# Kernel optimization log

Hardware: AMD Instinct MI355X
Metric: run time of the kernel (lower is better)

The kernel has to match this reference:

```python
import jax, jax.numpy as jnp
import numpy as np

B, N, D, D_MODEL = 4, 2048, 512, 512


def setup_inputs() -> dict:
    key = jax.random.key(0)
    kx, kq, kk, kv, ks = jax.random.split(key, 5)
    scale = 1.0 / np.sqrt(D)
    x = jax.random.normal(kx, (B, N, D), dtype=jnp.float32)
    Wq = (jax.random.normal(kq, (D, D_MODEL), dtype=jnp.float32) * scale)
    Wk = (jax.random.normal(kk, (D, D_MODEL), dtype=jnp.float32) * scale)
    Wv = (jax.random.normal(kv, (D, D_MODEL), dtype=jnp.float32) * scale)
    Ws = (jax.random.normal(ks, (D, 1), dtype=jnp.float32) * scale)
    return {"x": x, "Wq": Wq, "Wk": Wk, "Wv": Wv, "Ws": Ws}


def reference(x, Wq, Wk, Wv, Ws):
    # Projections (Linear, no bias)
    Q = x @ Wq                      # (B, N, d_model)
    K = x @ Wk                      # (B, N, d_model)
    V = x @ Wv                      # (B, N, d_model)
    sigma = x @ Ws                  # (B, N, 1)

    n = x.shape[1]
    dm = Wq.shape[1]

    # Prior association: Gaussian kernel over |i-j| distance, row-normalized
    idx = jnp.arange(n)
    dist = jnp.abs(idx[:, None] - idx[None, :]).astype(x.dtype)      # (N, N)
    inv_norm = 1.0 / (jnp.sqrt(2.0 * jnp.pi).astype(x.dtype) * jnp.abs(sigma))
    gaussian = inv_norm * jnp.exp(-0.5 * jnp.square(dist[None] / sigma))  # (B,N,N)
    P = gaussian / jnp.sum(gaussian, axis=-1, keepdims=True)

    # Series association: scaled dot-product softmax attention
    scores = jnp.einsum('bnd,bmd->bnm', Q, K) / jnp.sqrt(jnp.asarray(dm, x.dtype))
    S = jax.nn.softmax(scores, axis=-1)                               # (B,N,N)

    # Reconstruction
    Z = S @ V                                                          # (B,N,d_model)
    return (Z, P)
```

## Files before the change

### kernel.cpp

```cpp
#include <hip/hip_runtime.h>

typedef float f32x4 __attribute__((ext_vector_type(4)));
typedef short s16x8 __attribute__((ext_vector_type(8)));
typedef unsigned short us4 __attribute__((ext_vector_type(4)));

#define MFMA16(a, b, c) __builtin_amdgcn_mfma_f32_16x16x32_bf16(a, b, c, 0, 0, 0)

#define GLOAD_LDS16(gp, lp) __builtin_amdgcn_global_load_lds( \
    (__attribute__((address_space(1))) void*)(gp),            \
    (__attribute__((address_space(3))) void*)(lp), 16, 0, 0)

__device__ __forceinline__ unsigned short f2bf(float f) {
    union { float f; unsigned u; } v; v.f = f;
    unsigned r = v.u + 0x7fffu + ((v.u >> 16) & 1u);
    return (unsigned short)(r >> 16);
}

__device__ __forceinline__ void gemm_core256(
    const unsigned short* __restrict__ Ab, size_t Astride,
    const unsigned short* __restrict__ Bb, size_t Bstride,
    int K, unsigned short* sh, int t, f32x4 acc[8][4])
{
    const int w = t >> 6, lane = t & 63;
    const int c = lane & 15, quad = lane >> 4;
    const int arow = (w >> 2) * 128;
    const int brow = (w & 3) * 64;
    const int srow = t >> 2;
    const int scol = (t & 3) * 8;

    const unsigned short* ga = Ab + (size_t)srow * Astride + scol;
    const unsigned short* gb = Bb + (size_t)srow * Bstride + scol;
    const int ntil = K >> 5;

#define STAGE256(p, bbuf) do {                                      \
        unsigned short* nb = sh + (bbuf) * 16384;                   \
        int kk = (p) * 32;                                          \
        GLOAD_LDS16(ga + kk,                 nb + t * 8);           \
        GLOAD_LDS16(ga + kk + 128 * Astride, nb + 4096 + t * 8);    \
        GLOAD_LDS16(gb + kk,                 nb + 8192 + t * 8);    \
        GLOAD_LDS16(gb + kk + 128 * Bstride, nb + 12288 + t * 8);   \
    } while (0)

    STAGE256(0, 0);
    STAGE256(1, 1);

    int cur = 0;
    for (int i = 0; i < ntil; i++) {
        if (i + 1 < ntil) asm volatile("s_waitcnt vmcnt(4)" ::: "memory");
        else              asm volatile("s_waitcnt vmcnt(0)" ::: "memory");
        __builtin_amdgcn_s_barrier();
        __builtin_amdgcn_sched_barrier(0);

        const unsigned short* buf = sh + cur * 16384;
        s16x8 af[8], bf[4];
        #pragma unroll
        for (int q = 0; q < 8; q++)
            af[q] = *(const s16x8*)(buf + (arow + q * 16 + c) * 32 + quad * 8);
        #pragma unroll
        for (int q = 0; q < 4; q++)
            bf[q] = *(const s16x8*)(buf + 8192 + (brow + q * 16 + c) * 32 + quad * 8);

        asm volatile("s_waitcnt lgkmcnt(0)" ::: "memory");
        __builtin_amdgcn_sched_barrier(0);

        #pragma unroll
        for (int mt = 0; mt < 8; mt++)
            #pragma unroll
            for (int nt = 0; nt < 4; nt++)
                acc[mt][nt] = MFMA16(af[mt], bf[nt], acc[mt][nt]);

        __builtin_amdgcn_s_barrier();
        __builtin_amdgcn_sched_barrier(0);

        if (i + 2 < ntil) STAGE256(i + 2, cur);
        cur ^= 1;
    }
#undef STAGE256
}

__device__ __forceinline__ void prior_wave(
    const float* __restrict__ x, const float* __restrict__ wsv,
    float* __restrict__ pout, int row, int lane)
{
    const float4* xr = (const float4*)(x + (size_t)row * 512);
    const float4* wr = (const float4*)wsv;
    float4 a0 = xr[lane * 2],     b0 = wr[lane * 2];
    float4 a1 = xr[lane * 2 + 1], b1 = wr[lane * 2 + 1];
    float part = a0.x * b0.x + a0.y * b0.y + a0.z * b0.z + a0.w * b0.w
               + a1.x * b1.x + a1.y * b1.y + a1.z * b1.z + a1.w * b1.w;
    #pragma unroll
    for (int o = 32; o; o >>= 1) part += __shfl_xor(part, o, 64);
    float sigma = part;
    float inv2 = 0.5f / (sigma * sigma);

    int i = row & 2047;
    float g[32];
    float sum = 0.f;
    #pragma unroll
    for (int u = 0; u < 8; u++) {
        #pragma unroll
        for (int v = 0; v < 4; v++) {
            float d = (float)(u * 256 + lane * 4 + v - i);
            float e = __expf(-(d * d) * inv2);
            g[u * 4 + v] = e;
            sum += e;
        }
    }
    #pragma unroll
    for (int o = 32; o; o >>= 1) sum += __shfl_xor(sum, o, 64);
    float inv = 1.0f / sum;

    float4* pr = (float4*)(pout + (size_t)row * 2048);
    #pragma unroll
    for (int u = 0; u < 8; u++) {
        float4 o4 = { g[u * 4] * inv, g[u * 4 + 1] * inv,
                      g[u * 4 + 2] * inv, g[u * 4 + 3] * inv };
        pr[u * 64 + lane] = o4;
    }
}

__global__ __launch_bounds__(256) void k_convert(
    const float* __restrict__ x, const float* __restrict__ wq,
    const float* __restrict__ wk, const float* __restrict__ wv,
    unsigned short* __restrict__ xbf, unsigned short* __restrict__ wt)
{
    __shared__ __align__(16) unsigned short lt[64][72];

    int bid = blockIdx.x, t = threadIdx.x;
    if (bid < 4096) {
        int gid = bid * 256 + t;
        float4 v = ((const float4*)x)[gid];
        us4 o = { f2bf(v.x), f2bf(v.y), f2bf(v.z), f2bf(v.w) };
        ((us4*)xbf)[gid] = o;
    } else {
        int idx = bid - 4096;
        int w = idx >> 6;
        int tile = idx & 63;
        int tk = tile >> 3, tn = tile & 7;
        const float* src = ((w == 0) ? wq : (w == 1) ? wk : wv)
                         + (size_t)(tk * 64) * 512 + tn * 64;

        int row = t >> 2;
        int c0 = (t & 3) * 16;
        const float4* s = (const float4*)(src + (size_t)row * 512 + c0);
        #pragma unroll
        for (int q = 0; q < 4; q++) {
            float4 v = s[q];
            lt[c0 + q * 4 + 0][row] = f2bf(v.x);
            lt[c0 + q * 4 + 1][row] = f2bf(v.y);
            lt[c0 + q * 4 + 2][row] = f2bf(v.z);
            lt[c0 + q * 4 + 3][row] = f2bf(v.w);
        }
        __syncthreads();

        int n = t >> 2;
        int k0 = (t & 3) * 16;
        s16x8 a = *(const s16x8*)&lt[n][k0];
        s16x8 b = *(const s16x8*)&lt[n][k0 + 8];
        unsigned short* dst = wt + (((size_t)(w * 512 + tn * 64 + n)) << 9)
                                 + tk * 64 + k0;
        *(s16x8*)dst = a;
        *(s16x8*)(dst + 8) = b;
    }
}

__global__ __launch_bounds__(512, 2) void k_proj(
    const unsigned short* __restrict__ xbf, const unsigned short* __restrict__ wt,
    unsigned short* __restrict__ qbf, unsigned short* __restrict__ kbf,
    unsigned short* __restrict__ vtbf)
{
    __shared__ __align__(16) unsigned short sh[32768];

    int t = threadIdx.x;
    int mt_ = blockIdx.x / 6, nt_ = blockIdx.x % 6;
    int m0 = mt_ * 256, n0 = nt_ * 256;

    f32x4 acc[8][4] = {};
    gemm_core256(xbf + (size_t)m0 * 512, 512, wt + (size_t)n0 * 512, 512,
                 512, sh, t, acc);

    int w = t >> 6, lane = t & 63, c = lane & 15, quad = lane >> 4;
    int wr = w >> 2, wc = w & 3;
    int sel = nt_ >> 1;

    if (sel < 2) {
        unsigned short* dst = sel ? kbf : qbf;
        int ncol0 = n0 - sel * 512;
        #pragma unroll
        for (int mt = 0; mt < 8; mt++) {
            #pragma unroll
            for (int nt = 0; nt < 4; nt++) {
                int col = ncol0 + wc * 64 + nt * 16 + c;
                #pragma unroll
                for (int r = 0; r < 4; r++) {
                    int rw = m0 + wr * 128 + mt * 16 + quad * 4 + r;
                    dst[(size_t)rw * 512 + col] = f2bf(acc[mt][nt][r]);
                }
            }
        }
    } else {
        #pragma unroll
        for (int mt = 0; mt < 8; mt++) {
            int rw0 = m0 + wr * 128 + mt * 16 + quad * 4;
            int bb = rw0 >> 11, nn = rw0 & 2047;
            #pragma unroll
            for (int nt = 0; nt < 4; nt++) {
                int d = (n0 - 1024) + wc * 64 + nt * 16 + c;
                us4 pk = { f2bf(acc[mt][nt][0]), f2bf(acc[mt][nt][1]),
                           f2bf(acc[mt][nt][2]), f2bf(acc[mt][nt][3]) };
                *(us4*)(vtbf + ((size_t)(bb * 512 + d)) * 2048 + nn) = pk;
            }
        }
    }
}

__device__ __forceinline__ void score_body(
    const unsigned short* __restrict__ qbf, const unsigned short* __restrict__ kbf,
    unsigned short* __restrict__ pbf,
    int b, int m0, int n0, int t, unsigned short* sh)
{
    f32x4 acc[8][4] = {};
    gemm_core256(qbf + (size_t)(b * 2048 + m0) * 512, 512,
                 kbf + (size_t)(b * 2048 + n0) * 512, 512,
                 512, sh, t, acc);

    int w = t >> 6, lane = t & 63, c = lane & 15, quad = lane >> 4;
    int wr = w >> 2, wc = w & 3;
    const float scale = 0.044194173824159216f;

    #pragma unroll
    for (int mt = 0; mt < 8; mt++) {
        #pragma unroll
        for (int nt = 0; nt < 4; nt++) {
            int col = n0 + wc * 64 + nt * 16 + c;
            #pragma unroll
            for (int r = 0; r < 4; r++) {
                int row = m0 + wr * 128 + mt * 16 + quad * 4 + r;
                pbf[(size_t)(b * 2048 + row) * 2048 + col]
                    = f2bf(__expf(acc[mt][nt][r] * scale));
            }
        }
    }
}

__global__ __launch_bounds__(512, 2) void k_score_prior(
    const unsigned short* __restrict__ qbf, const unsigned short* __restrict__ kbf,
    unsigned short* __restrict__ pbf,
    const float* __restrict__ x, const float* __restrict__ wsv,
    float* __restrict__ pout)
{
    __shared__ __align__(16) unsigned short sh[32768];

    int bid = blockIdx.x, t = threadIdx.x;
    if (bid < 256) {
        int b = bid >> 6, r = bid & 63;
        score_body(qbf, kbf, pbf, b, ((r >> 3) & 7) * 256, (r & 7) * 256, t, sh);
    } else {
        int row = (bid - 256) * 8 + (t >> 6);
        prior_wave(x, wsv, pout, row, t & 63);
    }
}

__global__ __launch_bounds__(512, 2) void k_score(
    const unsigned short* __restrict__ qbf, const unsigned short* __restrict__ kbf,
    unsigned short* __restrict__ pbf)
{
    __shared__ __align__(16) unsigned short sh[32768];
    int bid = blockIdx.x;
    int b = bid >> 6, r = bid & 63;
    score_body(qbf, kbf, pbf, b, ((r >> 3) & 7) * 256, (r & 7) * 256,
               threadIdx.x, sh);
}

__global__ __launch_bounds__(256) void k_out(
    const unsigned short* __restrict__ pbf, const unsigned short* __restrict__ vtbf,
    float* __restrict__ zout)
{
    __shared__ __align__(16) unsigned short sh[12288];

    int t = threadIdx.x;
    int b = blockIdx.z;
    int m0 = blockIdx.x * 128, n0 = blockIdx.y * 64;

    const int wave = t >> 6, lane = t & 63;
    const int c = lane & 15, quad = lane >> 4;
    const int wm = (wave >> 1) * 64, wn = (wave & 1) * 32;
    const int srow = t >> 2;
    const int scol = (t & 3) * 8;

    const unsigned short* ga = pbf + (size_t)(b * 2048 + m0 + srow) * 2048 + scol;
    const unsigned short* gb = vtbf + (size_t)(b * 512 + n0 + srow) * 2048 + scol;

    s16x8 ones;
    #pragma unroll
    for (int i = 0; i < 8; i++) ones[i] = (short)0x3F80;

    f32x4 acc[4][2] = {};
    f32x4 accl[4] = {};

    GLOAD_LDS16(ga,                  sh + t * 8);
    GLOAD_LDS16(ga + 64 * 2048,      sh + 2048 + t * 8);
    GLOAD_LDS16(gb,                  sh + 4096 + t * 8);
    GLOAD_LDS16(ga + 32,             sh + 6144 + t * 8);
    GLOAD_LDS16(ga + 32 + 64 * 2048, sh + 6144 + 2048 + t * 8);
    GLOAD_LDS16(gb + 32,             sh + 6144 + 4096 + t * 8);

    int cur = 0;
    for (int k0 = 0; k0 < 2048; k0 += 32) {
        if (k0 + 32 < 2048) asm volatile("s_waitcnt vmcnt(3)" ::: "memory");
        else                asm volatile("s_waitcnt vmcnt(0)" ::: "memory");
        __builtin_amdgcn_s_barrier();
        __builtin_amdgcn_sched_barrier(0);

        const unsigned short* buf = sh + cur * 6144;
        s16x8 af[4], bf[2];
        #pragma unroll
        for (int i = 0; i < 4; i++)
            af[i] = *(const s16x8*)(buf + (wm + i * 16 + c) * 32 + quad * 8);
        #pragma unroll
        for (int i = 0; i < 2; i++)
            bf[i] = *(const s16x8*)(buf + 4096 + (wn + i * 16 + c) * 32 + quad * 8);

        asm volatile("s_waitcnt lgkmcnt(0)" ::: "memory");
        __builtin_amdgcn_sched_barrier(0);

        #pragma unroll
        for (int mt = 0; mt < 4; mt++) {
            #pragma unroll
            for (int nt = 0; nt < 2; nt++)
                acc[mt][nt] = MFMA16(af[mt], bf[nt], acc[mt][nt]);
            accl[mt] = MFMA16(af[mt], ones, accl[mt]);
        }

        __builtin_amdgcn_s_barrier();
        __builtin_amdgcn_sched_barrier(0);

        if (k0 + 64 < 2048) {
            unsigned short* nb = sh + cur * 6144;
            GLOAD_LDS16(ga + k0 + 64,             nb + t * 8);
            GLOAD_LDS16(ga + k0 + 64 + 64 * 2048, nb + 2048 + t * 8);
            GLOAD_LDS16(gb + k0 + 64,             nb + 4096 + t * 8);
        }
        cur ^= 1;
    }

    #pragma unroll
    for (int mt = 0; mt < 4; mt++) {
        #pragma unroll
        for (int r = 0; r < 4; r++) {
            int row = wm + mt * 16 + quad * 4 + r;
            float inv = 1.0f / accl[mt][r];
            #pragma unroll
            for (int nt = 0; nt < 2; nt++) {
                zout[(size_t)(b * 2048 + m0 + row) * 512 + n0 + wn + nt * 16 + c]
                    = acc[mt][nt][r] * inv;
            }
        }
    }
}

__global__ __launch_bounds__(512) void k_prior(
    const float* __restrict__ x, const float* __restrict__ wsv,
    float* __restrict__ pout)
{
    int row = blockIdx.x * 8 + (threadIdx.x >> 6);
    prior_wave(x, wsv, pout, row, threadIdx.x & 63);
}

extern "C" void kernel_launch(void* const* d_in, const int* in_sizes, int n_in,
                              void* d_out, int out_size, void* d_ws, size_t ws_size,
                              hipStream_t stream)
{
    const float* x  = (const float*)d_in[0];
    const float* wq = (const float*)d_in[1];
    const float* wk = (const float*)d_in[2];
    const float* wv = (const float*)d_in[3];
    const float* ws = (const float*)d_in[4];

    float* zout = (float*)d_out;
    float* pout = zout + (size_t)4 * 2048 * 512;

    const size_t need = ((size_t)4194304 + 786432 + 3 * 4194304 + 16777216) * 2;

    if (ws_size >= need) {
        unsigned short* base = (unsigned short*)d_ws;
        unsigned short* xbf  = base;
        unsigned short* wt   = xbf  + (size_t)4194304;
        unsigned short* qbf  = wt   + (size_t)786432;
        unsigned short* kbf  = qbf  + (size_t)4194304;
        unsigned short* vtbf = kbf  + (size_t)4194304;
        unsigned short* pbf  = vtbf + (size_t)4194304;

        k_convert<<<dim3(4288), dim3(256), 0, stream>>>(x, wq, wk, wv, xbf, wt);
        k_proj       <<<dim3(192),      dim3(512), 0, stream>>>(xbf, wt, qbf, kbf, vtbf);
        k_score_prior<<<dim3(1280),     dim3(512), 0, stream>>>(qbf, kbf, pbf, x, ws, pout);
        k_out        <<<dim3(16, 8, 4), dim3(256), 0, stream>>>(pbf, vtbf, zout);
    } else {
        unsigned short* base = (unsigned short*)pout;
        unsigned short* pbf  = base;
        unsigned short* qbf  = base + (size_t)16777216;
        unsigned short* kbf  = qbf  + (size_t)4194304;
        unsigned short* vtbf = kbf  + (size_t)4194304;
        unsigned short* xbf  = base;
        unsigned short* wt   = base + (size_t)4194304;

        k_convert<<<dim3(4288), dim3(256), 0, stream>>>(x, wq, wk, wv, xbf, wt);
        k_proj <<<dim3(192),      dim3(512), 0, stream>>>(xbf, wt, qbf, kbf, vtbf);
        k_score<<<dim3(256),      dim3(512), 0, stream>>>(qbf, kbf, pbf);
        k_out  <<<dim3(16, 8, 4), dim3(256), 0, stream>>>(pbf, vtbf, zout);
        k_prior<<<dim3(1024),     dim3(512), 0, stream>>>(x, ws, pout);
    }
}
```

Baseline: 191.4 us.

## Move prior computation into output GEMM launch and deepen its K pipeline

The prior-association work now runs in the same launch as the S@V output kernel instead of alongside the score GEMM. The score kernel is split back out on its own. The output kernel's main loop now consumes 64 K-elements per barrier pair: it double-buffers pairs of 32-wide slices and keeps two stages in flight, with LDS doubled to 48KB. The aim is fewer barriers per K step, better hiding of global-load latency, and letting the memory-bound prior fill idle CUs during the 512-block output GEMM. The larger LDS footprint may lower occupancy of the output kernel.

```diff
diff --git a/kernel.cpp b/kernel.cpp
--- a/kernel.cpp
+++ b/kernel.cpp
@@ -214,11 +214,17 @@
     }
 }
 
-__device__ __forceinline__ void score_body(
+__global__ __launch_bounds__(512, 2) void k_score(
     const unsigned short* __restrict__ qbf, const unsigned short* __restrict__ kbf,
-    unsigned short* __restrict__ pbf,
-    int b, int m0, int n0, int t, unsigned short* sh)
-{
+    unsigned short* __restrict__ pbf)
+{
+    __shared__ __align__(16) unsigned short sh[32768];
+
+    int t = threadIdx.x;
+    int bid = blockIdx.x;
+    int b = bid >> 6, r = bid & 63;
+    int m0 = ((r >> 3) & 7) * 256, n0 = (r & 7) * 256;
+
     f32x4 acc[8][4] = {};
     gemm_core256(qbf + (size_t)(b * 2048 + m0) * 512, 512,
                  kbf + (size_t)(b * 2048 + n0) * 512, 512,
@@ -234,54 +240,20 @@
         for (int nt = 0; nt < 4; nt++) {
             int col = n0 + wc * 64 + nt * 16 + c;
             #pragma unroll
-            for (int r = 0; r < 4; r++) {
-                int row = m0 + wr * 128 + mt * 16 + quad * 4 + r;
+            for (int r2 = 0; r2 < 4; r2++) {
+                int row = m0 + wr * 128 + mt * 16 + quad * 4 + r2;
                 pbf[(size_t)(b * 2048 + row) * 2048 + col]
-                    = f2bf(__expf(acc[mt][nt][r] * scale));
+                    = f2bf(__expf(acc[mt][nt][r2] * scale));
             }
         }
     }
 }
 
-__global__ __launch_bounds__(512, 2) void k_score_prior(
-    const unsigned short* __restrict__ qbf, const unsigned short* __restrict__ kbf,
-    unsigned short* __restrict__ pbf,
-    const float* __restrict__ x, const float* __restrict__ wsv,
-    float* __restrict__ pout)
-{
-    __shared__ __align__(16) unsigned short sh[32768];
-
-    int bid = blockIdx.x, t = threadIdx.x;
-    if (bid < 256) {
-        int b = bid >> 6, r = bid & 63;
-        score_body(qbf, kbf, pbf, b, ((r >> 3) & 7) * 256, (r & 7) * 256, t, sh);
-    } else {
-        int row = (bid - 256) * 8 + (t >> 6);
-        prior_wave(x, wsv, pout, row, t & 63);
-    }
-}
-
-__global__ __launch_bounds__(512, 2) void k_score(
-    const unsigned short* __restrict__ qbf, const unsigned short* __restrict__ kbf,
-    unsigned short* __restrict__ pbf)
-{
-    __shared__ __align__(16) unsigned short sh[32768];
-    int bid = blockIdx.x;
-    int b = bid >> 6, r = bid & 63;
-    score_body(qbf, kbf, pbf, b, ((r >> 3) & 7) * 256, (r & 7) * 256,
-               threadIdx.x, sh);
-}
-
-__global__ __launch_bounds__(256) void k_out(
+__device__ __forceinline__ void out_body(
     const unsigned short* __restrict__ pbf, const unsigned short* __restrict__ vtbf,
-    float* __restrict__ zout)
-{
-    __shared__ __align__(16) unsigned short sh[12288];
-
-    int t = threadIdx.x;
-    int b = blockIdx.z;
-    int m0 = blockIdx.x * 128, n0 = blockIdx.y * 64;
-
+    float* __restrict__ zout, int b, int m0, int n0, int t,
+    unsigned short* sh)
+{
     const int wave = t >> 6, lane = t & 63;
     const int c = lane & 15, quad = lane >> 4;
     const int wm = (wave >> 1) * 64, wn = (wave & 1) * 32;
@@ -298,28 +270,41 @@
     f32x4 acc[4][2] = {};
     f32x4 accl[4] = {};
 
-    GLOAD_LDS16(ga,                  sh + t * 8);
-    GLOAD_LDS16(ga + 64 * 2048,      sh + 2048 + t * 8);
-    GLOAD_LDS16(gb,                  sh + 4096 + t * 8);
-    GLOAD_LDS16(ga + 32,             sh + 6144 + t * 8);
-    GLOAD_LDS16(ga + 32 + 64 * 2048, sh + 6144 + 2048 + t * 8);
-    GLOAD_LDS16(gb + 32,             sh + 6144 + 4096 + t * 8);
+#define STAGEPAIR(p, bbuf) do {                                     \
+        unsigned short* nb = sh + (bbuf) * 12288;                   \
+        int kk = (p) * 64;                                          \
+        GLOAD_LDS16(ga + kk,             nb + t * 8);               \
+        GLOAD_LDS16(ga + kk + 64 * 2048, nb + 2048 + t * 8);        \
+        GLOAD_LDS16(gb + kk,             nb + 4096 + t * 8);        \
+        GLOAD_LDS16(ga + kk + 32,             nb + 6144 + t * 8);   \
+        GLOAD_LDS16(ga + kk + 32 + 64 * 2048, nb + 8192 + t * 8);   \
+        GLOAD_LDS16(gb + kk + 32,             nb + 10240 + t * 8);  \
+    } while (0)
+
+    STAGEPAIR(0, 0);
+    STAGEPAIR(1, 1);
 
     int cur = 0;
-    for (int k0 = 0; k0 < 2048; k0 += 32) {
-        if (k0 + 32 < 2048) asm volatile("s_waitcnt vmcnt(3)" ::: "memory");
-        else                asm volatile("s_waitcnt vmcnt(0)" ::: "memory");
+    for (int i = 0; i < 32; i++) {
+        if (i + 1 < 32) asm volatile("s_waitcnt vmcnt(6)" ::: "memory");
+        else            asm volatile("s_waitcnt vmcnt(0)" ::: "memory");
         __builtin_amdgcn_s_barrier();
         __builtin_amdgcn_sched_barrier(0);
 
-        const unsigned short* buf = sh + cur * 6144;
-        s16x8 af[4], bf[2];
-        #pragma unroll
-        for (int i = 0; i < 4; i++)
-            af[i] = *(const s16x8*)(buf + (wm + i * 16 + c) * 32 + quad * 8);
-        #pragma unroll
-        for (int i = 0; i < 2; i++)
-            bf[i] = *(const s16x8*)(buf + 4096 + (wn + i * 16 + c) * 32 + quad * 8);
+        const unsigned short* buf = sh + cur * 12288;
+        s16x8 a0[4], b0[2], a1[4], b1[2];
+        #pragma unroll
+        for (int q = 0; q < 4; q++)
+            a0[q] = *(const s16x8*)(buf + (wm + q * 16 + c) * 32 + quad * 8);
+        #pragma unroll
+        for (int q = 0; q < 2; q++)
+            b0[q] = *(const s16x8*)(buf + 4096 + (wn + q * 16 + c) * 32 + quad * 8);
+        #pragma unroll
+        for (int q = 0; q < 4; q++)
+            a1[q] = *(const s16x8*)(buf + 6144 + (wm + q * 16 + c) * 32 + quad * 8);
+        #pragma unroll
+        for (int q = 0; q < 2; q++)
+            b1[q] = *(const s16x8*)(buf + 10240 + (wn + q * 16 + c) * 32 + quad * 8);
 
         asm volatile("s_waitcnt lgkmcnt(0)" ::: "memory");
         __builtin_amdgcn_sched_barrier(0);
@@ -328,21 +313,24 @@
         for (int mt = 0; mt < 4; mt++) {
             #pragma unroll
             for (int nt = 0; nt < 2; nt++)
-                acc[mt][nt] = MFMA16(af[mt], bf[nt], acc[mt][nt]);
-            accl[mt] = MFMA16(af[mt], ones, accl[mt]);
+                acc[mt][nt] = MFMA16(a0[mt], b0[nt], acc[mt][nt]);
+            accl[mt] = MFMA16(a0[mt], ones, accl[mt]);
+        }
+        #pragma unroll
+        for (int mt = 0; mt < 4; mt++) {
+            #pragma unroll
+            for (int nt = 0; nt < 2; nt++)
+                acc[mt][nt] = MFMA16(a1[mt], b1[nt], acc[mt][nt]);
+            accl[mt] = MFMA16(a1[mt], ones, accl[mt]);
         }
 
         __builtin_amdgcn_s_barrier();
         __builtin_amdgcn_sched_barrier(0);
 
-        if (k0 + 64 < 2048) {
-            unsigned short* nb = sh + cur * 6144;
-            GLOAD_LDS16(ga + k0 + 64,             nb + t * 8);
-            GLOAD_LDS16(ga + k0 + 64 + 64 * 2048, nb + 2048 + t * 8);
-            GLOAD_LDS16(gb + k0 + 64,             nb + 4096 + t * 8);
-        }
+        if (i + 2 < 32) STAGEPAIR(i + 2, cur);
         cur ^= 1;
     }
+#undef STAGEPAIR
 
     #pragma unroll
     for (int mt = 0; mt < 4; mt++) {
@@ -359,11 +347,39 @@
     }
 }
 
-__global__ __launch_bounds__(512) void k_prior(
+__global__ __launch_bounds__(256) void k_out_prior(
+    const unsigned short* __restrict__ pbf, const unsigned short* __restrict__ vtbf,
+    float* __restrict__ zout,
     const float* __restrict__ x, const float* __restrict__ wsv,
     float* __restrict__ pout)
 {
-    int row = blockIdx.x * 8 + (threadIdx.x >> 6);
+    __shared__ __align__(16) unsigned short sh[24576];
+
+    int bid = blockIdx.x, t = threadIdx.x;
+    if (bid < 512) {
+        int b = bid >> 7, r = bid & 127;
+        out_body(pbf, vtbf, zout, b, (r >> 3) * 128, (r & 7) * 64, t, sh);
+    } else {
+        int row = (bid - 512) * 4 + (t >> 6);
+        prior_wave(x, wsv, pout, row, t & 63);
+    }
+}
+
+__global__ __launch_bounds__(256) void k_out(
+    const unsigned short* __restrict__ pbf, const unsigned short* __restrict__ vtbf,
+    float* __restrict__ zout)
+{
+    __shared__ __align__(16) unsigned short sh[24576];
+    int bid = blockIdx.x;
+    int b = bid >> 7, r = bid & 127;
+    out_body(pbf, vtbf, zout, b, (r >> 3) * 128, (r & 7) * 64, threadIdx.x, sh);
+}
+
+__global__ __launch_bounds__(256) void k_prior(
+    const float* __restrict__ x, const float* __restrict__ wsv,
+    float* __restrict__ pout)
+{
+    int row = blockIdx.x * 4 + (threadIdx.x >> 6);
     prior_wave(x, wsv, pout, row, threadIdx.x & 63);
 }
 
@@ -391,10 +407,10 @@
         unsigned short* vtbf = kbf  + (size_t)4194304;
         unsigned short* pbf  = vtbf + (size_t)4194304;
 
-        k_convert<<<dim3(4288), dim3(256), 0, stream>>>(x, wq, wk, wv, xbf, wt);
-        k_proj       <<<dim3(192),      dim3(512), 0, stream>>>(xbf, wt, qbf, kbf, vtbf);
-        k_score_prior<<<dim3(1280),     dim3(512), 0, stream>>>(qbf, kbf, pbf, x, ws, pout);
-        k_out        <<<dim3(16, 8, 4), dim3(256), 0, stream>>>(pbf, vtbf, zout);
+        k_convert  <<<dim3(4288), dim3(256), 0, stream>>>(x, wq, wk, wv, xbf, wt);
+        k_proj     <<<dim3(192),  dim3(512), 0, stream>>>(xbf, wt, qbf, kbf, vtbf);
+        k_score    <<<dim3(256),  dim3(512), 0, stream>>>(qbf, kbf, pbf);
+        k_out_prior<<<dim3(2560), dim3(256), 0, stream>>>(pbf, vtbf, zout, x, ws, pout);
     } else {
         unsigned short* base = (unsigned short*)pout;
         unsigned short* pbf  = base;
@@ -405,9 +421,9 @@
         unsigned short* wt   = base + (size_t)4194304;
 
         k_convert<<<dim3(4288), dim3(256), 0, stream>>>(x, wq, wk, wv, xbf, wt);
-        k_proj <<<dim3(192),      dim3(512), 0, stream>>>(xbf, wt, qbf, kbf, vtbf);
-        k_score<<<dim3(256),      dim3(512), 0, stream>>>(qbf, kbf, pbf);
-        k_out  <<<dim3(16, 8, 4), dim3(256), 0, stream>>>(pbf, vtbf, zout);
-        k_prior<<<dim3(1024),     dim3(512), 0, stream>>>(x, ws, pout);
-    }
-}
+        k_proj   <<<dim3(192),  dim3(512), 0, stream>>>(xbf, wt, qbf, kbf, vtbf);
+        k_score  <<<dim3(256),  dim3(512), 0, stream>>>(qbf, kbf, pbf);
+        k_out    <<<dim3(512),  dim3(256), 0, stream>>>(pbf, vtbf, zout);
+        k_prior  <<<dim3(2048), dim3(256), 0, stream>>>(x, ws, pout);
+    }
+}
```

Measured after the change: 193.7 us. About the same (+1.2%).
